# Performance work log

Measured on AMD Instinct MI355X. Metric: run time of the kernel, lower is better.

## Reference

```python
import jax, jax.numpy as jnp
import numpy as np


def _pairwise_upper_dists(x):
    # x: [N, D] -> distances for all i<j pairs, shape [N*(N-1)/2]
    n = x.shape[0]
    sq = jnp.sum(x * x, axis=-1)                      # [N]
    d2 = sq[:, None] + sq[None, :] - 2.0 * (x @ x.T)  # [N, N]
    d2 = jnp.maximum(d2, 0.0)
    iu, ju = jnp.triu_indices(n, k=1)                 # matches combinations(range(n), 2)
    return jnp.sqrt(d2[iu, ju])


def setup_inputs() -> dict:
    key = jax.random.key(0)
    k1, k2 = jax.random.split(key)
    pred = jax.random.normal(k1, (1024, 8192), dtype=jnp.float32)
    target = jax.random.normal(k2, (1024, 8192), dtype=jnp.float32)
    return {"pred": pred, "target": target}


def reference(pred, target):
    # all_pairs_in_batch=True branch: Euclidean distance per pair, MSE between
    # the pred-distance vector and the target-distance vector.
    pred_d = _pairwise_upper_dists(pred)      # [P]
    target_d = _pairwise_upper_dists(target)  # [P]
    return jnp.mean((pred_d - target_d) ** 2)
```

## Files before the change

kernel.cpp:

```cpp
#include <hip/hip_runtime.h>
#include <hip/hip_bf16.h>
#include <hip/hip_fp16.h>

#define D 8192
#define NPAIR 523776.0

typedef short short8 __attribute__((ext_vector_type(8)));
typedef float f32x4 __attribute__((ext_vector_type(4)));

__device__ __forceinline__ short8 cvt8(const float4 a, const float4 b) {
    union { short8 s; __hip_bfloat162 h[4]; } u;
    u.h[0] = __float22bfloat162_rn(make_float2(a.x, a.y));
    u.h[1] = __float22bfloat162_rn(make_float2(a.z, a.w));
    u.h[2] = __float22bfloat162_rn(make_float2(b.x, b.y));
    u.h[3] = __float22bfloat162_rn(make_float2(b.z, b.w));
    return u.s;
}

__device__ __forceinline__ void decode_bid(int bid, int& m, int& ti, int& tj, int& k0, int& nsteps) {
    int x = bid & 7, s = bid >> 3;
    m = x >> 2;
    int xr = x & 3;
    if (s < 16) {
        ti = tj = s & 7;
        int c = ((s >> 3) << 2) + xr;
        k0 = c * 1024; nsteps = 32;
    } else {
        int sp = s - 16;
        int c = (sp / 28) * 4 + xr;
        int tt = sp % 28;
        int a = 0;
        while (tt >= 7 - a) { tt -= 7 - a; ++a; }
        ti = a; tj = a + 1 + tt;
        k0 = c * 512; nsteps = 16;
    }
}
__device__ __forceinline__ int bid_off(int m, int tt, int c) {
    return (m * 4 + (c & 3)) + ((16 + (c >> 2) * 28 + tt) << 3);
}
__device__ __forceinline__ int bid_diag(int m, int dt, int c) {
    return (m * 4 + (c & 3)) + ((((c >> 2) << 3) + dt) << 3);
}

#define GRAM_STEP(S, RA, RB) { \
    const int cur_ = (S) & 1; \
    const short* __restrict__ bufA = lsA[cur_]; \
    const short* __restrict__ bufB = same ? lsA[cur_] : lsB[cur_]; \
    __builtin_amdgcn_s_setprio(1); \
    short8 bf0 = *(const short8*)((const char*)bufB + (rbB + kby)); \
    short8 bf1 = *(const short8*)((const char*)bufB + (rbB + 1024 + kby)); \
    _Pragma("unroll") \
    for (int mi = 0; mi < 4; ++mi) { \
        short8 af = *(const short8*)((const char*)bufA + (rbA + mi * 1024 + kby)); \
        acc[mi][0] = __builtin_amdgcn_mfma_f32_16x16x32_bf16(af, bf0, acc[mi][0], 0, 0, 0); \
        acc[mi][1] = __builtin_amdgcn_mfma_f32_16x16x32_bf16(af, bf1, acc[mi][1], 0, 0, 0); \
    } \
    __builtin_amdgcn_s_setprio(0); \
    if ((S) + 1 < nsteps) { \
        const int nxt_ = cur_ ^ 1; \
        *(short8*)((char*)lsA[nxt_] + wby) = cvt8(RA[0], RA[1]); \
        if (!same) *(short8*)((char*)lsB[nxt_] + wby) = cvt8(RB[0], RB[1]); \
        if ((S) + 3 < nsteps) { \
            const float4* p_ = (const float4*)(gA + ((S) + 3) * 32); \
            RA[0] = p_[0]; RA[1] = p_[1]; \
            if (!same) { \
                const float4* q_ = (const float4*)(gB + ((S) + 3) * 32); \
                RB[0] = q_[0]; RB[1] = q_[1]; \
            } \
        } \
    } \
    asm volatile("s_waitcnt lgkmcnt(0)" ::: "memory"); \
    __builtin_amdgcn_s_barrier(); \
}

template<bool STORE>
__global__ __launch_bounds__(512, 4)
void gram_kernel(const float* __restrict__ pred, const float* __restrict__ tgt,
                 void* __restrict__ outv, float* __restrict__ norms) {
    int m, ti, tj, k0, nsteps;
    decode_bid(blockIdx.x, m, ti, tj, k0, nsteps);
    const bool same = (ti == tj);
    const float* __restrict__ x = m ? tgt : pred;

    __shared__ short lsA[2][4096];
    __shared__ short lsB[2][4096];

    const int tid = threadIdx.x;
    const int lane = tid & 63;
    const int wid = tid >> 6;
    const int wr = wid >> 2, wc = wid & 3;

    const int srow = tid >> 2, sc8 = tid & 3;
    const float* __restrict__ gA = x + (size_t)(ti * 128 + srow) * D + k0 + sc8 * 8;
    const float* __restrict__ gB = x + (size_t)(tj * 128 + srow) * D + k0 + sc8 * 8;
    const int wby = srow * 64 + ((sc8 ^ ((srow >> 1) & 3)) << 4);

    const int rbA = (wr * 64 + (lane & 15)) * 64;
    const int rbB = (wc * 32 + (lane & 15)) * 64;
    const int kby = (((lane >> 4) ^ (((lane & 15) >> 1) & 3)) << 4);

    f32x4 zero = {0.f, 0.f, 0.f, 0.f};
    f32x4 acc[4][2];
#pragma unroll
    for (int mi = 0; mi < 4; ++mi) { acc[mi][0] = zero; acc[mi][1] = zero; }

    float4 raX[2], rbX[2], raY[2], rbY[2];

    { const float4* p = (const float4*)gA; raX[0] = p[0]; raX[1] = p[1];
      if (!same) { const float4* q = (const float4*)gB; rbX[0] = q[0]; rbX[1] = q[1]; } }
    *(short8*)((char*)lsA[0] + wby) = cvt8(raX[0], raX[1]);
    if (!same) *(short8*)((char*)lsB[0] + wby) = cvt8(rbX[0], rbX[1]);
    { const float4* p = (const float4*)(gA + 32); raX[0] = p[0]; raX[1] = p[1];
      if (!same) { const float4* q = (const float4*)(gB + 32); rbX[0] = q[0]; rbX[1] = q[1]; } }
    { const float4* p = (const float4*)(gA + 64); raY[0] = p[0]; raY[1] = p[1];
      if (!same) { const float4* q = (const float4*)(gB + 64); rbY[0] = q[0]; rbY[1] = q[1]; } }
    asm volatile("s_waitcnt lgkmcnt(0)" ::: "memory");
    __builtin_amdgcn_s_barrier();

    for (int sp = 0; sp < nsteps; sp += 2) {
        GRAM_STEP(sp,     raX, rbX)
        GRAM_STEP(sp + 1, raY, rbY)
    }

    if (STORE) {
        __half* __restrict__ dst = (__half*)outv + (size_t)blockIdx.x * 16384;
#pragma unroll
        for (int mi = 0; mi < 4; ++mi)
#pragma unroll
            for (int ni = 0; ni < 2; ++ni)
#pragma unroll
                for (int r = 0; r < 4; ++r) {
                    int li = wr * 64 + mi * 16 + (lane >> 4) * 4 + r;
                    int lj = wc * 32 + ni * 16 + (lane & 15);
                    dst[li * 128 + lj] = __float2half_rn(acc[mi][ni][r]);
                    if (same && li == lj)
                        atomicAdd(&norms[m * 1024 + ti * 128 + li], acc[mi][ni][r]);
                }
    } else {
        float* __restrict__ g = (float*)outv + (size_t)m * (1024 * 1024);
#pragma unroll
        for (int mi = 0; mi < 4; ++mi)
#pragma unroll
            for (int ni = 0; ni < 2; ++ni)
#pragma unroll
                for (int r = 0; r < 4; ++r) {
                    int gi = ti * 128 + wr * 64 + mi * 16 + (lane >> 4) * 4 + r;
                    int gj = tj * 128 + wc * 32 + ni * 16 + (lane & 15);
                    atomicAdd(&g[gi * 1024 + gj], acc[mi][ni][r]);
                }
    }
}

__global__ __launch_bounds__(256)
void loss_store_kernel(const __half* __restrict__ part, const float* __restrict__ norms,
                       float* __restrict__ partial) {
    const int tid = threadIdx.x;
    const int base = blockIdx.x * 256 + tid;
    float local = 0.f;
#pragma unroll
    for (int s = 0; s < 4; ++s) {
        int lin = base + s * 262144;
        int i = lin >> 10, j = lin & 1023;
        if (j > i) {
            int ti = i >> 7, tj = j >> 7;
            int el = ((i & 127) << 7) + (j & 127);
            float gp = 0.f, gt = 0.f;
            if (ti == tj) {
#pragma unroll
                for (int c = 0; c < 8; ++c) {
                    gp += __half2float(part[(size_t)bid_diag(0, ti, c) * 16384 + el]);
                    gt += __half2float(part[(size_t)bid_diag(1, ti, c) * 16384 + el]);
                }
            } else {
                int tt = 7 * ti - (ti * (ti - 1)) / 2 + (tj - ti - 1);
#pragma unroll
                for (int c = 0; c < 16; ++c) {
                    gp += __half2float(part[(size_t)bid_off(0, tt, c) * 16384 + el]);
                    gt += __half2float(part[(size_t)bid_off(1, tt, c) * 16384 + el]);
                }
            }
            float dp = norms[i] + norms[j] - 2.f * gp;
            float dt_ = norms[1024 + i] + norms[1024 + j] - 2.f * gt;
            float c2 = sqrtf(fmaxf(dp, 0.f)) - sqrtf(fmaxf(dt_, 0.f));
            local += c2 * c2;
        }
    }
#pragma unroll
    for (int off = 32; off > 0; off >>= 1) local += __shfl_down(local, off);
    __shared__ float wsum[4];
    if ((tid & 63) == 0) wsum[tid >> 6] = local;
    __syncthreads();
    if (tid == 0) partial[blockIdx.x] = wsum[0] + wsum[1] + wsum[2] + wsum[3];
}

__global__ __launch_bounds__(256)
void loss_atomic_kernel(const float* __restrict__ gram, float* __restrict__ partial) {
    const float* __restrict__ gP = gram;
    const float* __restrict__ gT = gram + 1024 * 1024;
    const int tid = threadIdx.x;
    const int base = blockIdx.x * 256 + tid;
    float local = 0.f;
#pragma unroll
    for (int s = 0; s < 4; ++s) {
        int lin = base + s * 262144;
        int i = lin >> 10, j = lin & 1023;
        if (j > i) {
            float dp = gP[i * 1024 + i] + gP[j * 1024 + j] - 2.f * gP[lin];
            float dt = gT[i * 1024 + i] + gT[j * 1024 + j] - 2.f * gT[lin];
            float c = sqrtf(fmaxf(dp, 0.f)) - sqrtf(fmaxf(dt, 0.f));
            local += c * c;
        }
    }
#pragma unroll
    for (int off = 32; off > 0; off >>= 1) local += __shfl_down(local, off);
    __shared__ float wsum[4];
    if ((tid & 63) == 0) wsum[tid >> 6] = local;
    __syncthreads();
    if (tid == 0) partial[blockIdx.x] = wsum[0] + wsum[1] + wsum[2] + wsum[3];
}

__global__ __launch_bounds__(256)
void finalize_kernel(const float* __restrict__ partial, float* __restrict__ out) {
    const int tid = threadIdx.x;
    double local = 0.0;
#pragma unroll
    for (int k = 0; k < 4; ++k) local += (double)partial[tid + k * 256];
#pragma unroll
    for (int off = 32; off > 0; off >>= 1) local += __shfl_down(local, off);
    __shared__ double wsum[4];
    if ((tid & 63) == 0) wsum[tid >> 6] = local;
    __syncthreads();
    if (tid == 0) out[0] = (float)((wsum[0] + wsum[1] + wsum[2] + wsum[3]) / NPAIR);
}

extern "C" void kernel_launch(void* const* d_in, const int* in_sizes, int n_in,
                              void* d_out, int out_size, void* d_ws, size_t ws_size,
                              hipStream_t stream) {
    const float* pred = (const float*)d_in[0];
    const float* tgt  = (const float*)d_in[1];
    const size_t part_bytes = (size_t)1024 * 16384 * sizeof(__half);
    const size_t need = part_bytes + (2048 + 1024) * sizeof(float);
    if (ws_size >= need) {
        __half* part   = (__half*)d_ws;
        float* norms   = (float*)((char*)d_ws + part_bytes);
        float* partial = norms + 2048;
        hipMemsetAsync(norms, 0, 2048 * sizeof(float), stream);
        gram_kernel<true><<<1024, 512, 0, stream>>>(pred, tgt, (void*)part, norms);
        loss_store_kernel<<<1024, 256, 0, stream>>>(part, norms, partial);
        finalize_kernel<<<1, 256, 0, stream>>>(partial, (float*)d_out);
    } else {
        float* gram    = (float*)d_ws;
        float* partial = (float*)d_ws + (size_t)2 * 1024 * 1024;
        hipMemsetAsync(gram, 0, (size_t)2 * 1024 * 1024 * sizeof(float), stream);
        gram_kernel<false><<<1024, 512, 0, stream>>>(pred, tgt, (void*)gram, nullptr);
        loss_atomic_kernel<<<1024, 256, 0, stream>>>(gram, partial);
        finalize_kernel<<<1, 256, 0, stream>>>(partial, (float*)d_out);
    }
}
```

Measured before the change: 54.51 us.

## Use 128x256 gram tiles covering the upper triangle with uniform K-splits

Replaces the 128x128 tile scheme (separate diagonal and off-diagonal tiles, with diagonal tiles using longer K ranges) with 128x256 tiles whose column strip is chosen so the tile set covers the upper triangle. Every block now runs a uniform 16-step K chunk with 16 K-splits, for 640 blocks instead of 1024. Each block loads B once for a 256-wide strip, which raises operand reuse per MFMA and reduces total global reads and partial stores. The cost is more accumulators, 48KB of LDS per block and a lower occupancy hint, and some blocks compute tile regions below the diagonal that are thrown away. The prefetch depth drops from two steps ahead to one.

```diff
diff --git a/kernel.cpp b/kernel.cpp
--- a/kernel.cpp
+++ b/kernel.cpp
@@ -4,6 +4,7 @@
 
 #define D 8192
 #define NPAIR 523776.0
+#define NSTEPS 16
 
 typedef short short8 __attribute__((ext_vector_type(8)));
 typedef float f32x4 __attribute__((ext_vector_type(4)));
@@ -17,56 +18,47 @@
     return u.s;
 }
 
-__device__ __forceinline__ void decode_bid(int bid, int& m, int& ti, int& tj, int& k0, int& nsteps) {
+__device__ __forceinline__ void decode_bid(int bid, int& m, int& ti, int& tjc, int& c) {
     int x = bid & 7, s = bid >> 3;
     m = x >> 2;
-    int xr = x & 3;
-    if (s < 16) {
-        ti = tj = s & 7;
-        int c = ((s >> 3) << 2) + xr;
-        k0 = c * 1024; nsteps = 32;
-    } else {
-        int sp = s - 16;
-        int c = (sp / 28) * 4 + xr;
-        int tt = sp % 28;
-        int a = 0;
-        while (tt >= 7 - a) { tt -= 7 - a; ++a; }
-        ti = a; tj = a + 1 + tt;
-        k0 = c * 512; nsteps = 16;
-    }
-}
-__device__ __forceinline__ int bid_off(int m, int tt, int c) {
-    return (m * 4 + (c & 3)) + ((16 + (c >> 2) * 28 + tt) << 3);
-}
-__device__ __forceinline__ int bid_diag(int m, int dt, int c) {
-    return (m * 4 + (c & 3)) + ((((c >> 2) << 3) + dt) << 3);
-}
-
-#define GRAM_STEP(S, RA, RB) { \
+    int t = s >> 2;
+    c = ((s & 3) << 2) + (x & 3);
+    if (t >= 12)      { tjc = 3; ti = t - 12; }
+    else if (t >= 6)  { tjc = 2; ti = t - 6; }
+    else if (t >= 2)  { tjc = 1; ti = t - 2; }
+    else              { tjc = 0; ti = t; }
+}
+__device__ __forceinline__ int bid_from(int m, int t, int c) {
+    return ((m << 2) + (c & 3)) + (((t << 2) + (c >> 2)) << 3);
+}
+
+#define GRAM_STEP(S) { \
     const int cur_ = (S) & 1; \
-    const short* __restrict__ bufA = lsA[cur_]; \
-    const short* __restrict__ bufB = same ? lsA[cur_] : lsB[cur_]; \
+    const char* __restrict__ buf = (const char*)ls[cur_]; \
     __builtin_amdgcn_s_setprio(1); \
-    short8 bf0 = *(const short8*)((const char*)bufB + (rbB + kby)); \
-    short8 bf1 = *(const short8*)((const char*)bufB + (rbB + 1024 + kby)); \
+    short8 bf0 = *(const short8*)(buf + rbB + kby); \
+    short8 bf1 = *(const short8*)(buf + rbB + 1024 + kby); \
+    short8 bf2 = *(const short8*)(buf + rbB + 2048 + kby); \
+    short8 bf3 = *(const short8*)(buf + rbB + 3072 + kby); \
     _Pragma("unroll") \
     for (int mi = 0; mi < 4; ++mi) { \
-        short8 af = *(const short8*)((const char*)bufA + (rbA + mi * 1024 + kby)); \
+        short8 af = *(const short8*)(buf + rbA + mi * 1024 + kby); \
         acc[mi][0] = __builtin_amdgcn_mfma_f32_16x16x32_bf16(af, bf0, acc[mi][0], 0, 0, 0); \
         acc[mi][1] = __builtin_amdgcn_mfma_f32_16x16x32_bf16(af, bf1, acc[mi][1], 0, 0, 0); \
+        acc[mi][2] = __builtin_amdgcn_mfma_f32_16x16x32_bf16(af, bf2, acc[mi][2], 0, 0, 0); \
+        acc[mi][3] = __builtin_amdgcn_mfma_f32_16x16x32_bf16(af, bf3, acc[mi][3], 0, 0, 0); \
     } \
     __builtin_amdgcn_s_setprio(0); \
-    if ((S) + 1 < nsteps) { \
-        const int nxt_ = cur_ ^ 1; \
-        *(short8*)((char*)lsA[nxt_] + wby) = cvt8(RA[0], RA[1]); \
-        if (!same) *(short8*)((char*)lsB[nxt_] + wby) = cvt8(RB[0], RB[1]); \
-        if ((S) + 3 < nsteps) { \
-            const float4* p_ = (const float4*)(gA + ((S) + 3) * 32); \
-            RA[0] = p_[0]; RA[1] = p_[1]; \
-            if (!same) { \
-                const float4* q_ = (const float4*)(gB + ((S) + 3) * 32); \
-                RB[0] = q_[0]; RB[1] = q_[1]; \
-            } \
+    if ((S) + 1 < NSTEPS) { \
+        char* __restrict__ nb = (char*)ls[cur_ ^ 1]; \
+        *(short8*)(nb + wbyA)  = cvt8(ra[0], ra[1]); \
+        *(short8*)(nb + wbyB0) = cvt8(rb[0], rb[1]); \
+        *(short8*)(nb + wbyB1) = cvt8(rb[2], rb[3]); \
+        if ((S) + 2 < NSTEPS) { \
+            const float4* pa_ = (const float4*)(gA + ((S) + 2) * 32); \
+            ra[0] = pa_[0]; ra[1] = pa_[1]; \
+            const float4* pb_ = (const float4*)(gB + ((S) + 2) * 32); \
+            rb[0] = pb_[0]; rb[1] = pb_[1]; rb[2] = pb_[2]; rb[3] = pb_[3]; \
         } \
     } \
     asm volatile("s_waitcnt lgkmcnt(0)" ::: "memory"); \
@@ -74,66 +66,70 @@
 }
 
 template<bool STORE>
-__global__ __launch_bounds__(512, 4)
+__global__ __launch_bounds__(512, 3)
 void gram_kernel(const float* __restrict__ pred, const float* __restrict__ tgt,
                  void* __restrict__ outv, float* __restrict__ norms) {
-    int m, ti, tj, k0, nsteps;
-    decode_bid(blockIdx.x, m, ti, tj, k0, nsteps);
-    const bool same = (ti == tj);
+    int m, ti, tjc, c;
+    decode_bid(blockIdx.x, m, ti, tjc, c);
     const float* __restrict__ x = m ? tgt : pred;
-
-    __shared__ short lsA[2][4096];
-    __shared__ short lsB[2][4096];
+    const int k0 = c * 512;
+
+    __shared__ short ls[2][12288];
 
     const int tid = threadIdx.x;
     const int lane = tid & 63;
     const int wid = tid >> 6;
     const int wr = wid >> 2, wc = wid & 3;
 
-    const int srow = tid >> 2, sc8 = tid & 3;
-    const float* __restrict__ gA = x + (size_t)(ti * 128 + srow) * D + k0 + sc8 * 8;
-    const float* __restrict__ gB = x + (size_t)(tj * 128 + srow) * D + k0 + sc8 * 8;
-    const int wby = srow * 64 + ((sc8 ^ ((srow >> 1) & 3)) << 4);
+    const int arow = tid >> 2, aslot = tid & 3;
+    const float* __restrict__ gA = x + (size_t)(ti * 128 + arow) * D + k0 + aslot * 8;
+    const int wbyA = arow * 64 + ((aslot ^ ((arow >> 1) & 3)) << 4);
+    const int brow = tid >> 1, bs0 = (tid & 1) << 1;
+    const float* __restrict__ gB = x + (size_t)(tjc * 256 + brow) * D + k0 + bs0 * 8;
+    const int wbyB0 = 8192 + brow * 64 + (((bs0)     ^ ((brow >> 1) & 3)) << 4);
+    const int wbyB1 = 8192 + brow * 64 + (((bs0 | 1) ^ ((brow >> 1) & 3)) << 4);
 
     const int rbA = (wr * 64 + (lane & 15)) * 64;
-    const int rbB = (wc * 32 + (lane & 15)) * 64;
+    const int rbB = 8192 + (wc * 64 + (lane & 15)) * 64;
     const int kby = (((lane >> 4) ^ (((lane & 15) >> 1) & 3)) << 4);
 
     f32x4 zero = {0.f, 0.f, 0.f, 0.f};
-    f32x4 acc[4][2];
-#pragma unroll
-    for (int mi = 0; mi < 4; ++mi) { acc[mi][0] = zero; acc[mi][1] = zero; }
-
-    float4 raX[2], rbX[2], raY[2], rbY[2];
-
-    { const float4* p = (const float4*)gA; raX[0] = p[0]; raX[1] = p[1];
-      if (!same) { const float4* q = (const float4*)gB; rbX[0] = q[0]; rbX[1] = q[1]; } }
-    *(short8*)((char*)lsA[0] + wby) = cvt8(raX[0], raX[1]);
-    if (!same) *(short8*)((char*)lsB[0] + wby) = cvt8(rbX[0], rbX[1]);
-    { const float4* p = (const float4*)(gA + 32); raX[0] = p[0]; raX[1] = p[1];
-      if (!same) { const float4* q = (const float4*)(gB + 32); rbX[0] = q[0]; rbX[1] = q[1]; } }
-    { const float4* p = (const float4*)(gA + 64); raY[0] = p[0]; raY[1] = p[1];
-      if (!same) { const float4* q = (const float4*)(gB + 64); rbY[0] = q[0]; rbY[1] = q[1]; } }
+    f32x4 acc[4][4];
+#pragma unroll
+    for (int mi = 0; mi < 4; ++mi)
+#pragma unroll
+        for (int ni = 0; ni < 4; ++ni) acc[mi][ni] = zero;
+
+    float4 ra[2], rb[4];
+    { const float4* pa = (const float4*)gA; ra[0] = pa[0]; ra[1] = pa[1];
+      const float4* pb = (const float4*)gB; rb[0] = pb[0]; rb[1] = pb[1]; rb[2] = pb[2]; rb[3] = pb[3]; }
+    *(short8*)((char*)ls[0] + wbyA)  = cvt8(ra[0], ra[1]);
+    *(short8*)((char*)ls[0] + wbyB0) = cvt8(rb[0], rb[1]);
+    *(short8*)((char*)ls[0] + wbyB1) = cvt8(rb[2], rb[3]);
+    { const float4* pa = (const float4*)(gA + 32); ra[0] = pa[0]; ra[1] = pa[1];
+      const float4* pb = (const float4*)(gB + 32); rb[0] = pb[0]; rb[1] = pb[1]; rb[2] = pb[2]; rb[3] = pb[3]; }
     asm volatile("s_waitcnt lgkmcnt(0)" ::: "memory");
     __builtin_amdgcn_s_barrier();
 
-    for (int sp = 0; sp < nsteps; sp += 2) {
-        GRAM_STEP(sp,     raX, rbX)
-        GRAM_STEP(sp + 1, raY, rbY)
-    }
-
+#pragma unroll
+    for (int sp = 0; sp < NSTEPS; sp += 2) {
+        GRAM_STEP(sp)
+        GRAM_STEP(sp + 1)
+    }
+
+    const bool straddle = ((ti >> 1) == tjc);
     if (STORE) {
-        __half* __restrict__ dst = (__half*)outv + (size_t)blockIdx.x * 16384;
+        __half* __restrict__ dst = (__half*)outv + (size_t)blockIdx.x * 32768;
 #pragma unroll
         for (int mi = 0; mi < 4; ++mi)
 #pragma unroll
-            for (int ni = 0; ni < 2; ++ni)
+            for (int ni = 0; ni < 4; ++ni)
 #pragma unroll
                 for (int r = 0; r < 4; ++r) {
                     int li = wr * 64 + mi * 16 + (lane >> 4) * 4 + r;
-                    int lj = wc * 32 + ni * 16 + (lane & 15);
-                    dst[li * 128 + lj] = __float2half_rn(acc[mi][ni][r]);
-                    if (same && li == lj)
+                    int lj = wc * 64 + ni * 16 + (lane & 15);
+                    dst[li * 256 + lj] = __float2half_rn(acc[mi][ni][r]);
+                    if (straddle && lj == (((ti & 1) << 7) + li))
                         atomicAdd(&norms[m * 1024 + ti * 128 + li], acc[mi][ni][r]);
                 }
     } else {
@@ -141,12 +137,12 @@
 #pragma unroll
         for (int mi = 0; mi < 4; ++mi)
 #pragma unroll
-            for (int ni = 0; ni < 2; ++ni)
+            for (int ni = 0; ni < 4; ++ni)
 #pragma unroll
                 for (int r = 0; r < 4; ++r) {
                     int gi = ti * 128 + wr * 64 + mi * 16 + (lane >> 4) * 4 + r;
-                    int gj = tj * 128 + wc * 32 + ni * 16 + (lane & 15);
-                    atomicAdd(&g[gi * 1024 + gj], acc[mi][ni][r]);
+                    int gj = tjc * 256 + wc * 64 + ni * 16 + (lane & 15);
+                    if (gj >= gi) atomicAdd(&g[gi * 1024 + gj], acc[mi][ni][r]);
                 }
     }
 }
@@ -162,22 +158,14 @@
         int lin = base + s * 262144;
         int i = lin >> 10, j = lin & 1023;
         if (j > i) {
-            int ti = i >> 7, tj = j >> 7;
-            int el = ((i & 127) << 7) + (j & 127);
+            int ti = i >> 7, tjc = j >> 8;
+            int t = tjc * (tjc + 1) + ti;
+            int el = ((i & 127) << 8) + (j & 255);
             float gp = 0.f, gt = 0.f;
-            if (ti == tj) {
-#pragma unroll
-                for (int c = 0; c < 8; ++c) {
-                    gp += __half2float(part[(size_t)bid_diag(0, ti, c) * 16384 + el]);
-                    gt += __half2float(part[(size_t)bid_diag(1, ti, c) * 16384 + el]);
-                }
-            } else {
-                int tt = 7 * ti - (ti * (ti - 1)) / 2 + (tj - ti - 1);
-#pragma unroll
-                for (int c = 0; c < 16; ++c) {
-                    gp += __half2float(part[(size_t)bid_off(0, tt, c) * 16384 + el]);
-                    gt += __half2float(part[(size_t)bid_off(1, tt, c) * 16384 + el]);
-                }
+#pragma unroll
+            for (int c = 0; c < 16; ++c) {
+                gp += __half2float(part[(size_t)bid_from(0, t, c) * 32768 + el]);
+                gt += __half2float(part[(size_t)bid_from(1, t, c) * 32768 + el]);
             }
             float dp = norms[i] + norms[j] - 2.f * gp;
             float dt_ = norms[1024 + i] + norms[1024 + j] - 2.f * gt;
@@ -238,21 +226,21 @@
                               hipStream_t stream) {
     const float* pred = (const float*)d_in[0];
     const float* tgt  = (const float*)d_in[1];
-    const size_t part_bytes = (size_t)1024 * 16384 * sizeof(__half);
-    const size_t need = part_bytes + (2048 + 1024) * sizeof(float);
+    const size_t part_halves = (size_t)640 * 32768;
+    const size_t need = part_halves * sizeof(__half) + (2048 + 1024) * sizeof(float);
     if (ws_size >= need) {
         __half* part   = (__half*)d_ws;
-        float* norms   = (float*)((char*)d_ws + part_bytes);
+        float* norms   = (float*)((char*)d_ws + part_halves * sizeof(__half));
         float* partial = norms + 2048;
         hipMemsetAsync(norms, 0, 2048 * sizeof(float), stream);
-        gram_kernel<true><<<1024, 512, 0, stream>>>(pred, tgt, (void*)part, norms);
+        gram_kernel<true><<<640, 512, 0, stream>>>(pred, tgt, (void*)part, norms);
         loss_store_kernel<<<1024, 256, 0, stream>>>(part, norms, partial);
         finalize_kernel<<<1, 256, 0, stream>>>(partial, (float*)d_out);
     } else {
         float* gram    = (float*)d_ws;
         float* partial = (float*)d_ws + (size_t)2 * 1024 * 1024;
         hipMemsetAsync(gram, 0, (size_t)2 * 1024 * 1024 * sizeof(float), stream);
-        gram_kernel<false><<<1024, 512, 0, stream>>>(pred, tgt, (void*)gram, nullptr);
+        gram_kernel<false><<<640, 512, 0, stream>>>(pred, tgt, (void*)gram, nullptr);
         loss_atomic_kernel<<<1024, 256, 0, stream>>>(gram, partial);
         finalize_kernel<<<1, 256, 0, stream>>>(partial, (float*)d_out);
     }
```

Result: slower. 66.57 us (+22.1%).
